# Kernel optimization log

Measured on AMD Instinct MI355X. Metric: run time of the kernel, lower is better.

## Reference

```python
import jax, jax.numpy as jnp
import numpy as np

N = 100000
IN_C = 256
HID = 128


def setup_inputs() -> dict:
    key = jax.random.key(0)
    ks = jax.random.split(key, 8)
    x = jax.random.normal(ks[0], (N, IN_C), dtype=jnp.float32)
    edge_index = jax.random.randint(ks[1], (2, 1600000), 0, N, dtype=jnp.int64)
    # GCNConv: lin (bias=False) + separate additive bias
    W1 = jax.random.normal(ks[2], (IN_C, HID), dtype=jnp.float32) / np.sqrt(IN_C)
    b1 = jnp.zeros((HID,), dtype=jnp.float32)
    W2 = jax.random.normal(ks[3], (HID, HID // 2), dtype=jnp.float32) / np.sqrt(HID)
    b2 = jnp.zeros((HID // 2,), dtype=jnp.float32)
    Wfc = jax.random.normal(ks[4], (HID // 2, 2), dtype=jnp.float32) / np.sqrt(HID // 2)
    bfc = jnp.zeros((2,), dtype=jnp.float32)
    return {"x": x, "edge_index": edge_index, "W1": W1, "b1": b1,
            "W2": W2, "b2": b2, "Wfc": Wfc, "bfc": bfc}


def _gcn_norm(edge_index, n):
    # add self-loops, symmetric normalization (PyG gcn_norm defaults)
    loop = jnp.arange(n, dtype=edge_index.dtype)
    src = jnp.concatenate([edge_index[0], loop])
    dst = jnp.concatenate([edge_index[1], loop])
    deg = jax.ops.segment_sum(jnp.ones_like(src, dtype=jnp.float32), dst,
                              num_segments=n)
    dinv = jnp.where(deg > 0, jax.lax.rsqrt(deg), 0.0)
    norm = dinv[src] * dinv[dst]  # [E + N]
    return src, dst, norm


def _gcn_conv(x, W, b, src, dst, norm, n):
    h = x @ W                       # [N, out] dense transform first
    msg = h[src] * norm[:, None]    # irregular gather, [E+N, out]
    out = jax.ops.segment_sum(msg, dst, num_segments=n)  # scatter-add
    return out + b


def reference(x, edge_index, W1, b1, W2, b2, Wfc, bfc):
    n = x.shape[0]
    src, dst, norm = _gcn_norm(edge_index, n)
    h = jax.nn.relu(_gcn_conv(x, W1, b1, src, dst, norm, n))
    # dropout is identity in eval mode
    h = jax.nn.relu(_gcn_conv(h, W2, b2, src, dst, norm, n))
    logits = h @ Wfc + bfc  # [N, 2]
    return jax.nn.log_softmax(logits, axis=1)
```

## Files before the change

### kernel.cpp

```cpp
#include <hip/hip_runtime.h>
#include <math.h>

#define IN_C 256
#define HID 128
#define H2  64
#define CAP 64

typedef __attribute__((ext_vector_type(8))) short bf16x8;
typedef __attribute__((ext_vector_type(4))) float f32x4;

__device__ __forceinline__ unsigned short f2bf(float f) {
  union { float f; unsigned int u; } v; v.f = f;
  unsigned int r = v.u + 0x7FFFu + ((v.u >> 16) & 1u);
  return (unsigned short)(r >> 16);
}
__device__ __forceinline__ float bf_lo(unsigned int u) {
  union { unsigned int u; float f; } v; v.u = u << 16; return v.f;
}
__device__ __forceinline__ float bf_hi(unsigned int u) {
  union { unsigned int u; float f; } v; v.u = u & 0xffff0000u; return v.f;
}
__device__ __forceinline__ unsigned int pack_bf(float lo, float hi) {
  return (unsigned int)f2bf(lo) | ((unsigned int)f2bf(hi) << 16);
}

__global__ void wcast_kernel(const float* __restrict__ W, unsigned short* __restrict__ Wt,
                             int K, int N) {
  int idx = blockIdx.x * 256 + threadIdx.x;
  if (idx < K * N) {
    int nn = idx / K, kk = idx % K;
    Wt[idx] = f2bf(W[kk * N + nn]);
  }
}

__global__ void dinv_kernel(const int* __restrict__ fill, float* __restrict__ dinv, int n) {
  int i = blockIdx.x * 256 + threadIdx.x;
  if (i < n) dinv[i] = rsqrtf((float)(fill[i] + 1));
}

template <int K, int N, int BM, int WM, int WN, bool A_BF16, bool SCALE>
__device__ __forceinline__ void gemm_body(const void* __restrict__ Av,
                                          const unsigned short* __restrict__ Bt,
                                          const float* __restrict__ dinv,
                                          unsigned short* __restrict__ C, int M,
                                          int bidx, short* As, short* Bs) {
  constexpr int WTM = BM / WM;
  constexpr int WTN = N / WN;
  constexpr int MB = WTM / 16, NB = WTN / 16;
  constexpr int ACH = BM * 4 / 256;
  constexpr int BCH = N * 4 / 256;

  int tid = threadIdx.x;
  int lane = tid & 63, wid = tid >> 6;
  int ln15 = lane & 15, kg = lane >> 4;
  int wm = wid / WN, wn = wid % WN;
  int row0 = bidx * BM;

  f32x4 acc[MB][NB];
#pragma unroll
  for (int i = 0; i < MB; ++i)
#pragma unroll
    for (int j = 0; j < NB; ++j) acc[i][j] = (f32x4)0.0f;

  for (int k0 = 0; k0 < K; k0 += 32) {
#pragma unroll
    for (int p = 0; p < ACH; ++p) {
      int c = p * 256 + tid;
      int row = c >> 2, kc = c & 3;
      int grow = row0 + row;
      if (A_BF16) {
        const unsigned short* Ab = (const unsigned short*)Av;
        uint4 v = make_uint4(0, 0, 0, 0);
        if (grow < M) v = *reinterpret_cast<const uint4*>(&Ab[(size_t)grow * K + k0 + kc * 8]);
        *reinterpret_cast<uint4*>(&As[row * 40 + kc * 8]) = v;
      } else {
        const float* A = (const float*)Av;
        float4 v0 = make_float4(0.f, 0.f, 0.f, 0.f), v1 = v0;
        if (grow < M) {
          const float4* ap = reinterpret_cast<const float4*>(&A[(size_t)grow * K + k0 + kc * 8]);
          v0 = ap[0]; v1 = ap[1];
        }
        bf16x8 w;
        w[0] = (short)f2bf(v0.x); w[1] = (short)f2bf(v0.y);
        w[2] = (short)f2bf(v0.z); w[3] = (short)f2bf(v0.w);
        w[4] = (short)f2bf(v1.x); w[5] = (short)f2bf(v1.y);
        w[6] = (short)f2bf(v1.z); w[7] = (short)f2bf(v1.w);
        *reinterpret_cast<bf16x8*>(&As[row * 40 + kc * 8]) = w;
      }
    }
#pragma unroll
    for (int p = 0; p < BCH; ++p) {
      int c = p * 256 + tid;
      int nrow = c >> 2, kc = c & 3;
      *reinterpret_cast<uint4*>(&Bs[nrow * 40 + kc * 8]) =
          *reinterpret_cast<const uint4*>(&Bt[(size_t)nrow * K + k0 + kc * 8]);
    }
    __syncthreads();
    bf16x8 af[MB], bfr[NB];
#pragma unroll
    for (int mb = 0; mb < MB; ++mb)
      af[mb] = *reinterpret_cast<const bf16x8*>(&As[(wm * WTM + mb * 16 + ln15) * 40 + kg * 8]);
#pragma unroll
    for (int nb = 0; nb < NB; ++nb)
      bfr[nb] = *reinterpret_cast<const bf16x8*>(&Bs[(wn * WTN + nb * 16 + ln15) * 40 + kg * 8]);
#pragma unroll
    for (int mb = 0; mb < MB; ++mb)
#pragma unroll
      for (int nb = 0; nb < NB; ++nb)
        acc[mb][nb] = __builtin_amdgcn_mfma_f32_16x16x32_bf16(af[mb], bfr[nb], acc[mb][nb], 0, 0, 0);
    __syncthreads();
  }
#pragma unroll
  for (int mb = 0; mb < MB; ++mb)
#pragma unroll
    for (int nb = 0; nb < NB; ++nb) {
      int gcol = wn * WTN + nb * 16 + ln15;
#pragma unroll
      for (int q = 0; q < 4; ++q) {
        int grow = row0 + wm * WTM + mb * 16 + kg * 4 + q;
        if (grow < M) {
          float v = acc[mb][nb][q];
          if (SCALE) v *= dinv[grow];
          C[(size_t)grow * N + gcol] = f2bf(v);
        }
      }
    }
}

__global__ __launch_bounds__(256) void fused_g1_place(
    const float* __restrict__ x, const unsigned short* __restrict__ W1T,
    unsigned short* __restrict__ h1lin, int M,
    const int* __restrict__ src, const int* __restrict__ dst, int E,
    int* __restrict__ fill, int* __restrict__ col, int GB, int PB) {
  __shared__ short smem[(64 + HID) * 40];
  int bid = blockIdx.x;
  int gp = GB < PB ? GB : PB;
  int m2 = 2 * gp;
  bool isPlace; int idx;
  if (bid < m2) { isPlace = (bid & 1); idx = bid >> 1; }
  else          { isPlace = (PB > GB); idx = gp + (bid - m2); }

  if (!isPlace) {
    gemm_body<IN_C, HID, 64, 2, 2, false, false>(x, W1T, nullptr, h1lin, M, idx,
                                                 smem, smem + 64 * 40);
  } else {
    int tid = threadIdx.x;
    int base = idx * 1024;
    int ee[4], dd[4], ss[4], sl[4]; bool ok[4];
#pragma unroll
    for (int j = 0; j < 4; ++j) { ee[j] = base + j * 256 + tid; ok[j] = ee[j] < E; }
#pragma unroll
    for (int j = 0; j < 4; ++j) {
      dd[j] = ok[j] ? dst[ee[j]] : 0;
      ss[j] = ok[j] ? src[ee[j]] : 0;
    }
#pragma unroll
    for (int j = 0; j < 4; ++j)
      sl[j] = ok[j] ? atomicAdd(&fill[dd[j]], 1) : CAP;
#pragma unroll
    for (int j = 0; j < 4; ++j)
      if (ok[j] && sl[j] < CAP) col[(size_t)dd[j] * CAP + sl[j]] = ss[j];
  }
}

__global__ __launch_bounds__(256) void gemm2_kernel(const unsigned short* __restrict__ A,
                                                    const unsigned short* __restrict__ Bt,
                                                    unsigned short* __restrict__ C, int M) {
  __shared__ short smem[(64 + H2) * 40];
  gemm_body<HID, H2, 64, 2, 2, true, false>(A, Bt, nullptr, C, M, blockIdx.x,
                                            smem, smem + 64 * 40);
}

__global__ __launch_bounds__(256) void agg1_kernel(const uint2* __restrict__ hs,
    const int* __restrict__ fill, const int* __restrict__ col,
    const float* __restrict__ dinv, const float* __restrict__ bias,
    uint2* __restrict__ outb, int n) {
  int sub = threadIdx.x >> 5, l = threadIdx.x & 31;
  int i = blockIdx.x * 8 + sub;
  if (i >= n) return;
  float di = dinv[i];
  int cnt = fill[i]; cnt = cnt > CAP ? CAP : cnt;
  const int* cp = col + (size_t)i * CAP;
  uint2 us = hs[(size_t)i * 32 + l];
  float a0 = di * bf_lo(us.x), a1 = di * bf_hi(us.x);
  float a2 = di * bf_lo(us.y), a3 = di * bf_hi(us.y);
  int k = 0;
  for (; k + 7 < cnt; k += 8) {
    int c[8]; float w[8]; uint2 u[8];
#pragma unroll
    for (int j = 0; j < 8; ++j) c[j] = cp[k + j];
#pragma unroll
    for (int j = 0; j < 8; ++j) { w[j] = dinv[c[j]]; u[j] = hs[(size_t)c[j] * 32 + l]; }
#pragma unroll
    for (int j = 0; j < 8; ++j) {
      a0 += w[j] * bf_lo(u[j].x); a1 += w[j] * bf_hi(u[j].x);
      a2 += w[j] * bf_lo(u[j].y); a3 += w[j] * bf_hi(u[j].y);
    }
  }
  for (; k + 3 < cnt; k += 4) {
    int c[4]; float w[4]; uint2 u[4];
#pragma unroll
    for (int j = 0; j < 4; ++j) c[j] = cp[k + j];
#pragma unroll
    for (int j = 0; j < 4; ++j) { w[j] = dinv[c[j]]; u[j] = hs[(size_t)c[j] * 32 + l]; }
#pragma unroll
    for (int j = 0; j < 4; ++j) {
      a0 += w[j] * bf_lo(u[j].x); a1 += w[j] * bf_hi(u[j].x);
      a2 += w[j] * bf_lo(u[j].y); a3 += w[j] * bf_hi(u[j].y);
    }
  }
  for (; k < cnt; ++k) {
    int c = cp[k]; float w = dinv[c];
    uint2 u = hs[(size_t)c * 32 + l];
    a0 += w * bf_lo(u.x); a1 += w * bf_hi(u.x);
    a2 += w * bf_lo(u.y); a3 += w * bf_hi(u.y);
  }
  float4 b = reinterpret_cast<const float4*>(bias)[l];
  a0 = di * fmaxf(di * a0 + b.x, 0.f);
  a1 = di * fmaxf(di * a1 + b.y, 0.f);
  a2 = di * fmaxf(di * a2 + b.z, 0.f);
  a3 = di * fmaxf(di * a3 + b.w, 0.f);
  uint2 o; o.x = pack_bf(a0, a1); o.y = pack_bf(a2, a3);
  outb[(size_t)i * 32 + l] = o;
}

__global__ __launch_bounds__(256) void agg2fc_kernel(const uint2* __restrict__ hs,
    const int* __restrict__ fill, const int* __restrict__ col,
    const float* __restrict__ dinv, const float* __restrict__ bias,
    const float* __restrict__ Wfc, const float* __restrict__ bfc,
    float* __restrict__ out, int n) {
  int sub = threadIdx.x >> 4, l = threadIdx.x & 15;
  int i = blockIdx.x * 16 + sub;
  if (i >= n) return;
  float di = dinv[i];
  int cnt = fill[i]; cnt = cnt > CAP ? CAP : cnt;
  const int* cp = col + (size_t)i * CAP;
  uint2 us = hs[(size_t)i * 16 + l];
  float a0 = bf_lo(us.x), a1 = bf_hi(us.x), a2 = bf_lo(us.y), a3 = bf_hi(us.y);
  int k = 0;
  for (; k + 7 < cnt; k += 8) {
    int c[8]; uint2 u[8];
#pragma unroll
    for (int j = 0; j < 8; ++j) c[j] = cp[k + j];
#pragma unroll
    for (int j = 0; j < 8; ++j) u[j] = hs[(size_t)c[j] * 16 + l];
#pragma unroll
    for (int j = 0; j < 8; ++j) {
      a0 += bf_lo(u[j].x); a1 += bf_hi(u[j].x);
      a2 += bf_lo(u[j].y); a3 += bf_hi(u[j].y);
    }
  }
  for (; k + 1 < cnt; k += 2) {
    uint2 u0 = hs[(size_t)cp[k] * 16 + l];
    uint2 u1 = hs[(size_t)cp[k + 1] * 16 + l];
    a0 += bf_lo(u0.x) + bf_lo(u1.x); a1 += bf_hi(u0.x) + bf_hi(u1.x);
    a2 += bf_lo(u0.y) + bf_lo(u1.y); a3 += bf_hi(u0.y) + bf_hi(u1.y);
  }
  if (k < cnt) {
    uint2 u = hs[(size_t)cp[k] * 16 + l];
    a0 += bf_lo(u.x); a1 += bf_hi(u.x); a2 += bf_lo(u.y); a3 += bf_hi(u.y);
  }
  float4 b = reinterpret_cast<const float4*>(bias)[l];
  a0 = fmaxf(di * a0 + b.x, 0.f);
  a1 = fmaxf(di * a1 + b.y, 0.f);
  a2 = fmaxf(di * a2 + b.z, 0.f);
  a3 = fmaxf(di * a3 + b.w, 0.f);
  float4 w01 = reinterpret_cast<const float4*>(Wfc)[2 * l];
  float4 w23 = reinterpret_cast<const float4*>(Wfc)[2 * l + 1];
  float p0 = a0 * w01.x + a1 * w01.z + a2 * w23.x + a3 * w23.z;
  float p1 = a0 * w01.y + a1 * w01.w + a2 * w23.y + a3 * w23.w;
#pragma unroll
  for (int off = 8; off; off >>= 1) {
    p0 += __shfl_xor(p0, off, 16);
    p1 += __shfl_xor(p1, off, 16);
  }
  if (l == 0) {
    float l0 = p0 + bfc[0], l1 = p1 + bfc[1];
    float m = fmaxf(l0, l1);
    float lse = m + logf(expf(l0 - m) + expf(l1 - m));
    float2 o; o.x = l0 - lse; o.y = l1 - lse;
    reinterpret_cast<float2*>(out)[i] = o;
  }
}

extern "C" void kernel_launch(void* const* d_in, const int* in_sizes, int n_in,
                              void* d_out, int out_size, void* d_ws, size_t ws_size,
                              hipStream_t stream) {
  const float* x   = (const float*)d_in[0];
  const int*   ei  = (const int*)d_in[1];
  const float* W1  = (const float*)d_in[2];
  const float* b1  = (const float*)d_in[3];
  const float* W2  = (const float*)d_in[4];
  const float* b2  = (const float*)d_in[5];
  const float* Wfc = (const float*)d_in[6];
  const float* bfc = (const float*)d_in[7];
  float* out = (float*)d_out;

  int n = in_sizes[0] / IN_C;
  int E = in_sizes[1] / 2;
  const int* src = ei;
  const int* dst = ei + E;

  char* ws = (char*)d_ws;
  size_t off = 0;
  auto alloc = [&](size_t bytes) {
    void* p = ws + off;
    off = (off + bytes + 255) & ~(size_t)255;
    return p;
  };
  int*   fill   = (int*)alloc((size_t)n * 4);
  float* dinv   = (float*)alloc((size_t)n * 4);
  int*   col    = (int*)alloc((size_t)n * CAP * 4);
  unsigned short* h1lin = (unsigned short*)alloc((size_t)n * HID * 2);
  unsigned short* h1    = (unsigned short*)alloc((size_t)n * HID * 2);
  unsigned short* h2lin = (unsigned short*)alloc((size_t)n * H2 * 2);
  unsigned short* W1T   = (unsigned short*)alloc((size_t)IN_C * HID * 2);
  unsigned short* W2T   = (unsigned short*)alloc((size_t)HID * H2 * 2);

  hipMemsetAsync(fill, 0, (size_t)n * 4, stream);
  wcast_kernel<<<(IN_C * HID + 255) / 256, 256, 0, stream>>>(W1, W1T, IN_C, HID);
  wcast_kernel<<<(HID * H2 + 255) / 256, 256, 0, stream>>>(W2, W2T, HID, H2);

  int GB = (n + 63) / 64;
  int PB = (E + 1023) / 1024;
  fused_g1_place<<<GB + PB, 256, 0, stream>>>(x, W1T, h1lin, n, src, dst, E, fill, col, GB, PB);

  dinv_kernel<<<(n + 255) / 256, 256, 0, stream>>>(fill, dinv, n);
  agg1_kernel<<<(n + 7) / 8, 256, 0, stream>>>((const uint2*)h1lin, fill, col, dinv, b1, (uint2*)h1, n);
  gemm2_kernel<<<(n + 63) / 64, 256, 0, stream>>>(h1, W2T, h2lin, n);
  agg2fc_kernel<<<(n + 15) / 16, 256, 0, stream>>>((const uint2*)h2lin, fill, col, dinv, b2, Wfc, bfc, out, n);
}
```

Before: 196.0 us.

## Widen aggregation loads to 16B, inline dinv, rebalance GEMM/placement block mix

Both aggregation kernels now read eight bf16 values per lane with uint4 loads, using half as many lanes per node and twice as many nodes per block. The separate dinv kernel and its buffer are removed; each node's normalization is computed on the fly as rsqrt(fill+1), including for every neighbour. The fused GEMM1 and edge-placement launch now interleaves four GEMM blocks with one placement block, and each placement block handles 4096 edges. The intent is fewer launches, wider memory transactions and better overlap of the atomic-heavy placement with the GEMM, at the cost of an extra gathered fill load and rsqrt per neighbour.

```diff
diff --git a/kernel.cpp b/kernel.cpp
--- a/kernel.cpp
+++ b/kernel.cpp
@@ -22,6 +22,18 @@
 }
 __device__ __forceinline__ unsigned int pack_bf(float lo, float hi) {
   return (unsigned int)f2bf(lo) | ((unsigned int)f2bf(hi) << 16);
+}
+__device__ __forceinline__ void add8w(float* a, uint4 u, float w) {
+  a[0] += w * bf_lo(u.x); a[1] += w * bf_hi(u.x);
+  a[2] += w * bf_lo(u.y); a[3] += w * bf_hi(u.y);
+  a[4] += w * bf_lo(u.z); a[5] += w * bf_hi(u.z);
+  a[6] += w * bf_lo(u.w); a[7] += w * bf_hi(u.w);
+}
+__device__ __forceinline__ void add8(float* a, uint4 u) {
+  a[0] += bf_lo(u.x); a[1] += bf_hi(u.x);
+  a[2] += bf_lo(u.y); a[3] += bf_hi(u.y);
+  a[4] += bf_lo(u.z); a[5] += bf_hi(u.z);
+  a[6] += bf_lo(u.w); a[7] += bf_hi(u.w);
 }
 
 __global__ void wcast_kernel(const float* __restrict__ W, unsigned short* __restrict__ Wt,
@@ -33,15 +45,9 @@
   }
 }
 
-__global__ void dinv_kernel(const int* __restrict__ fill, float* __restrict__ dinv, int n) {
-  int i = blockIdx.x * 256 + threadIdx.x;
-  if (i < n) dinv[i] = rsqrtf((float)(fill[i] + 1));
-}
-
-template <int K, int N, int BM, int WM, int WN, bool A_BF16, bool SCALE>
+template <int K, int N, int BM, int WM, int WN, bool A_BF16>
 __device__ __forceinline__ void gemm_body(const void* __restrict__ Av,
                                           const unsigned short* __restrict__ Bt,
-                                          const float* __restrict__ dinv,
                                           unsigned short* __restrict__ C, int M,
                                           int bidx, short* As, short* Bs) {
   constexpr int WTM = BM / WM;
@@ -118,11 +124,7 @@
 #pragma unroll
       for (int q = 0; q < 4; ++q) {
         int grow = row0 + wm * WTM + mb * 16 + kg * 4 + q;
-        if (grow < M) {
-          float v = acc[mb][nb][q];
-          if (SCALE) v *= dinv[grow];
-          C[(size_t)grow * N + gcol] = f2bf(v);
-        }
+        if (grow < M) C[(size_t)grow * N + gcol] = f2bf(acc[mb][nb][q]);
       }
     }
 }
@@ -134,31 +136,29 @@
     int* __restrict__ fill, int* __restrict__ col, int GB, int PB) {
   __shared__ short smem[(64 + HID) * 40];
   int bid = blockIdx.x;
-  int gp = GB < PB ? GB : PB;
-  int m2 = 2 * gp;
-  bool isPlace; int idx;
-  if (bid < m2) { isPlace = (bid & 1); idx = bid >> 1; }
-  else          { isPlace = (PB > GB); idx = gp + (bid - m2); }
-
+  bool isPlace = (bid % 5 == 4);
   if (!isPlace) {
-    gemm_body<IN_C, HID, 64, 2, 2, false, false>(x, W1T, nullptr, h1lin, M, idx,
-                                                 smem, smem + 64 * 40);
+    int idx = bid - bid / 5;
+    if (idx < GB)
+      gemm_body<IN_C, HID, 64, 2, 2, false>(x, W1T, h1lin, M, idx, smem, smem + 64 * 40);
   } else {
+    int idx = bid / 5;
+    if (idx >= PB) return;
     int tid = threadIdx.x;
-    int base = idx * 1024;
-    int ee[4], dd[4], ss[4], sl[4]; bool ok[4];
-#pragma unroll
-    for (int j = 0; j < 4; ++j) { ee[j] = base + j * 256 + tid; ok[j] = ee[j] < E; }
-#pragma unroll
-    for (int j = 0; j < 4; ++j) {
-      dd[j] = ok[j] ? dst[ee[j]] : 0;
-      ss[j] = ok[j] ? src[ee[j]] : 0;
+    int base = idx * 4096;
+    int dd[16], ss[16], sl[16]; bool ok[16];
+#pragma unroll
+    for (int j = 0; j < 16; ++j) {
+      int e = base + j * 256 + tid;
+      ok[j] = e < E;
+      dd[j] = ok[j] ? dst[e] : 0;
+      ss[j] = ok[j] ? src[e] : 0;
     }
 #pragma unroll
-    for (int j = 0; j < 4; ++j)
+    for (int j = 0; j < 16; ++j)
       sl[j] = ok[j] ? atomicAdd(&fill[dd[j]], 1) : CAP;
 #pragma unroll
-    for (int j = 0; j < 4; ++j)
+    for (int j = 0; j < 16; ++j)
       if (ok[j] && sl[j] < CAP) col[(size_t)dd[j] * CAP + sl[j]] = ss[j];
   }
 }
@@ -167,112 +167,124 @@
                                                     const unsigned short* __restrict__ Bt,
                                                     unsigned short* __restrict__ C, int M) {
   __shared__ short smem[(64 + H2) * 40];
-  gemm_body<HID, H2, 64, 2, 2, true, false>(A, Bt, nullptr, C, M, blockIdx.x,
-                                            smem, smem + 64 * 40);
-}
-
-__global__ __launch_bounds__(256) void agg1_kernel(const uint2* __restrict__ hs,
+  gemm_body<HID, H2, 64, 2, 2, true>(A, Bt, C, M, blockIdx.x, smem, smem + 64 * 40);
+}
+
+__global__ __launch_bounds__(256) void agg1_kernel(const uint4* __restrict__ hs4,
     const int* __restrict__ fill, const int* __restrict__ col,
-    const float* __restrict__ dinv, const float* __restrict__ bias,
-    uint2* __restrict__ outb, int n) {
-  int sub = threadIdx.x >> 5, l = threadIdx.x & 31;
-  int i = blockIdx.x * 8 + sub;
-  if (i >= n) return;
-  float di = dinv[i];
-  int cnt = fill[i]; cnt = cnt > CAP ? CAP : cnt;
-  const int* cp = col + (size_t)i * CAP;
-  uint2 us = hs[(size_t)i * 32 + l];
-  float a0 = di * bf_lo(us.x), a1 = di * bf_hi(us.x);
-  float a2 = di * bf_lo(us.y), a3 = di * bf_hi(us.y);
-  int k = 0;
-  for (; k + 7 < cnt; k += 8) {
-    int c[8]; float w[8]; uint2 u[8];
-#pragma unroll
-    for (int j = 0; j < 8; ++j) c[j] = cp[k + j];
-#pragma unroll
-    for (int j = 0; j < 8; ++j) { w[j] = dinv[c[j]]; u[j] = hs[(size_t)c[j] * 32 + l]; }
-#pragma unroll
-    for (int j = 0; j < 8; ++j) {
-      a0 += w[j] * bf_lo(u[j].x); a1 += w[j] * bf_hi(u[j].x);
-      a2 += w[j] * bf_lo(u[j].y); a3 += w[j] * bf_hi(u[j].y);
-    }
-  }
-  for (; k + 3 < cnt; k += 4) {
-    int c[4]; float w[4]; uint2 u[4];
-#pragma unroll
-    for (int j = 0; j < 4; ++j) c[j] = cp[k + j];
-#pragma unroll
-    for (int j = 0; j < 4; ++j) { w[j] = dinv[c[j]]; u[j] = hs[(size_t)c[j] * 32 + l]; }
-#pragma unroll
-    for (int j = 0; j < 4; ++j) {
-      a0 += w[j] * bf_lo(u[j].x); a1 += w[j] * bf_hi(u[j].x);
-      a2 += w[j] * bf_lo(u[j].y); a3 += w[j] * bf_hi(u[j].y);
-    }
-  }
-  for (; k < cnt; ++k) {
-    int c = cp[k]; float w = dinv[c];
-    uint2 u = hs[(size_t)c * 32 + l];
-    a0 += w * bf_lo(u.x); a1 += w * bf_hi(u.x);
-    a2 += w * bf_lo(u.y); a3 += w * bf_hi(u.y);
-  }
-  float4 b = reinterpret_cast<const float4*>(bias)[l];
-  a0 = di * fmaxf(di * a0 + b.x, 0.f);
-  a1 = di * fmaxf(di * a1 + b.y, 0.f);
-  a2 = di * fmaxf(di * a2 + b.z, 0.f);
-  a3 = di * fmaxf(di * a3 + b.w, 0.f);
-  uint2 o; o.x = pack_bf(a0, a1); o.y = pack_bf(a2, a3);
-  outb[(size_t)i * 32 + l] = o;
-}
-
-__global__ __launch_bounds__(256) void agg2fc_kernel(const uint2* __restrict__ hs,
-    const int* __restrict__ fill, const int* __restrict__ col,
-    const float* __restrict__ dinv, const float* __restrict__ bias,
-    const float* __restrict__ Wfc, const float* __restrict__ bfc,
-    float* __restrict__ out, int n) {
+    const float* __restrict__ bias, uint4* __restrict__ outb, int n) {
   int sub = threadIdx.x >> 4, l = threadIdx.x & 15;
   int i = blockIdx.x * 16 + sub;
   if (i >= n) return;
-  float di = dinv[i];
-  int cnt = fill[i]; cnt = cnt > CAP ? CAP : cnt;
+  int degi = fill[i];
+  float di = rsqrtf((float)(degi + 1));
+  int cnt = degi > CAP ? CAP : degi;
   const int* cp = col + (size_t)i * CAP;
-  uint2 us = hs[(size_t)i * 16 + l];
-  float a0 = bf_lo(us.x), a1 = bf_hi(us.x), a2 = bf_lo(us.y), a3 = bf_hi(us.y);
+  float a[8];
+  uint4 us = hs4[(size_t)i * 16 + l];
+  a[0] = di * bf_lo(us.x); a[1] = di * bf_hi(us.x);
+  a[2] = di * bf_lo(us.y); a[3] = di * bf_hi(us.y);
+  a[4] = di * bf_lo(us.z); a[5] = di * bf_hi(us.z);
+  a[6] = di * bf_lo(us.w); a[7] = di * bf_hi(us.w);
   int k = 0;
   for (; k + 7 < cnt; k += 8) {
-    int c[8]; uint2 u[8];
+    int c[8], f[8]; uint4 u[8];
 #pragma unroll
     for (int j = 0; j < 8; ++j) c[j] = cp[k + j];
 #pragma unroll
-    for (int j = 0; j < 8; ++j) u[j] = hs[(size_t)c[j] * 16 + l];
-#pragma unroll
-    for (int j = 0; j < 8; ++j) {
-      a0 += bf_lo(u[j].x); a1 += bf_hi(u[j].x);
-      a2 += bf_lo(u[j].y); a3 += bf_hi(u[j].y);
-    }
-  }
-  for (; k + 1 < cnt; k += 2) {
-    uint2 u0 = hs[(size_t)cp[k] * 16 + l];
-    uint2 u1 = hs[(size_t)cp[k + 1] * 16 + l];
-    a0 += bf_lo(u0.x) + bf_lo(u1.x); a1 += bf_hi(u0.x) + bf_hi(u1.x);
-    a2 += bf_lo(u0.y) + bf_lo(u1.y); a3 += bf_hi(u0.y) + bf_hi(u1.y);
-  }
-  if (k < cnt) {
-    uint2 u = hs[(size_t)cp[k] * 16 + l];
-    a0 += bf_lo(u.x); a1 += bf_hi(u.x); a2 += bf_lo(u.y); a3 += bf_hi(u.y);
-  }
-  float4 b = reinterpret_cast<const float4*>(bias)[l];
-  a0 = fmaxf(di * a0 + b.x, 0.f);
-  a1 = fmaxf(di * a1 + b.y, 0.f);
-  a2 = fmaxf(di * a2 + b.z, 0.f);
-  a3 = fmaxf(di * a3 + b.w, 0.f);
-  float4 w01 = reinterpret_cast<const float4*>(Wfc)[2 * l];
-  float4 w23 = reinterpret_cast<const float4*>(Wfc)[2 * l + 1];
-  float p0 = a0 * w01.x + a1 * w01.z + a2 * w23.x + a3 * w23.z;
-  float p1 = a0 * w01.y + a1 * w01.w + a2 * w23.y + a3 * w23.w;
-#pragma unroll
-  for (int off = 8; off; off >>= 1) {
-    p0 += __shfl_xor(p0, off, 16);
-    p1 += __shfl_xor(p1, off, 16);
+    for (int j = 0; j < 8; ++j) { f[j] = fill[c[j]]; u[j] = hs4[(size_t)c[j] * 16 + l]; }
+#pragma unroll
+    for (int j = 0; j < 8; ++j) add8w(a, u[j], rsqrtf((float)(f[j] + 1)));
+  }
+  for (; k + 3 < cnt; k += 4) {
+    int c[4], f[4]; uint4 u[4];
+#pragma unroll
+    for (int j = 0; j < 4; ++j) c[j] = cp[k + j];
+#pragma unroll
+    for (int j = 0; j < 4; ++j) { f[j] = fill[c[j]]; u[j] = hs4[(size_t)c[j] * 16 + l]; }
+#pragma unroll
+    for (int j = 0; j < 4; ++j) add8w(a, u[j], rsqrtf((float)(f[j] + 1)));
+  }
+  for (; k < cnt; ++k) {
+    int c = cp[k];
+    float w = rsqrtf((float)(fill[c] + 1));
+    add8w(a, hs4[(size_t)c * 16 + l], w);
+  }
+  float4 bA = reinterpret_cast<const float4*>(bias)[2 * l];
+  float4 bB = reinterpret_cast<const float4*>(bias)[2 * l + 1];
+  float r0 = di * fmaxf(di * a[0] + bA.x, 0.f);
+  float r1 = di * fmaxf(di * a[1] + bA.y, 0.f);
+  float r2 = di * fmaxf(di * a[2] + bA.z, 0.f);
+  float r3 = di * fmaxf(di * a[3] + bA.w, 0.f);
+  float r4 = di * fmaxf(di * a[4] + bB.x, 0.f);
+  float r5 = di * fmaxf(di * a[5] + bB.y, 0.f);
+  float r6 = di * fmaxf(di * a[6] + bB.z, 0.f);
+  float r7 = di * fmaxf(di * a[7] + bB.w, 0.f);
+  uint4 o;
+  o.x = pack_bf(r0, r1); o.y = pack_bf(r2, r3);
+  o.z = pack_bf(r4, r5); o.w = pack_bf(r6, r7);
+  outb[(size_t)i * 16 + l] = o;
+}
+
+__global__ __launch_bounds__(256) void agg2fc_kernel(const uint4* __restrict__ hs4,
+    const int* __restrict__ fill, const int* __restrict__ col,
+    const float* __restrict__ bias, const float* __restrict__ Wfc,
+    const float* __restrict__ bfc, float* __restrict__ out, int n) {
+  int sub = threadIdx.x >> 3, l = threadIdx.x & 7;
+  int i = blockIdx.x * 32 + sub;
+  if (i >= n) return;
+  int degi = fill[i];
+  float di = rsqrtf((float)(degi + 1));
+  int cnt = degi > CAP ? CAP : degi;
+  const int* cp = col + (size_t)i * CAP;
+  float a[8];
+  uint4 us = hs4[(size_t)i * 8 + l];
+  a[0] = bf_lo(us.x); a[1] = bf_hi(us.x);
+  a[2] = bf_lo(us.y); a[3] = bf_hi(us.y);
+  a[4] = bf_lo(us.z); a[5] = bf_hi(us.z);
+  a[6] = bf_lo(us.w); a[7] = bf_hi(us.w);
+  int k = 0;
+  for (; k + 7 < cnt; k += 8) {
+    int c[8]; uint4 u[8];
+#pragma unroll
+    for (int j = 0; j < 8; ++j) c[j] = cp[k + j];
+#pragma unroll
+    for (int j = 0; j < 8; ++j) u[j] = hs4[(size_t)c[j] * 8 + l];
+#pragma unroll
+    for (int j = 0; j < 8; ++j) add8(a, u[j]);
+  }
+  for (; k + 3 < cnt; k += 4) {
+    int c[4]; uint4 u[4];
+#pragma unroll
+    for (int j = 0; j < 4; ++j) c[j] = cp[k + j];
+#pragma unroll
+    for (int j = 0; j < 4; ++j) u[j] = hs4[(size_t)c[j] * 8 + l];
+#pragma unroll
+    for (int j = 0; j < 4; ++j) add8(a, u[j]);
+  }
+  for (; k < cnt; ++k) add8(a, hs4[(size_t)cp[k] * 8 + l]);
+  float4 bA = reinterpret_cast<const float4*>(bias)[2 * l];
+  float4 bB = reinterpret_cast<const float4*>(bias)[2 * l + 1];
+  float r[8];
+  r[0] = fmaxf(di * a[0] + bA.x, 0.f);
+  r[1] = fmaxf(di * a[1] + bA.y, 0.f);
+  r[2] = fmaxf(di * a[2] + bA.z, 0.f);
+  r[3] = fmaxf(di * a[3] + bA.w, 0.f);
+  r[4] = fmaxf(di * a[4] + bB.x, 0.f);
+  r[5] = fmaxf(di * a[5] + bB.y, 0.f);
+  r[6] = fmaxf(di * a[6] + bB.z, 0.f);
+  r[7] = fmaxf(di * a[7] + bB.w, 0.f);
+  float p0 = 0.f, p1 = 0.f;
+#pragma unroll
+  for (int s = 0; s < 4; ++s) {
+    float4 w = reinterpret_cast<const float4*>(Wfc)[4 * l + s];
+    p0 += r[2 * s] * w.x + r[2 * s + 1] * w.z;
+    p1 += r[2 * s] * w.y + r[2 * s + 1] * w.w;
+  }
+#pragma unroll
+  for (int off = 4; off; off >>= 1) {
+    p0 += __shfl_xor(p0, off, 8);
+    p1 += __shfl_xor(p1, off, 8);
   }
   if (l == 0) {
     float l0 = p0 + bfc[0], l1 = p1 + bfc[1];
@@ -309,7 +321,6 @@
     return p;
   };
   int*   fill   = (int*)alloc((size_t)n * 4);
-  float* dinv   = (float*)alloc((size_t)n * 4);
   int*   col    = (int*)alloc((size_t)n * CAP * 4);
   unsigned short* h1lin = (unsigned short*)alloc((size_t)n * HID * 2);
   unsigned short* h1    = (unsigned short*)alloc((size_t)n * HID * 2);
@@ -322,11 +333,11 @@
   wcast_kernel<<<(HID * H2 + 255) / 256, 256, 0, stream>>>(W2, W2T, HID, H2);
 
   int GB = (n + 63) / 64;
-  int PB = (E + 1023) / 1024;
-  fused_g1_place<<<GB + PB, 256, 0, stream>>>(x, W1T, h1lin, n, src, dst, E, fill, col, GB, PB);
-
-  dinv_kernel<<<(n + 255) / 256, 256, 0, stream>>>(fill, dinv, n);
-  agg1_kernel<<<(n + 7) / 8, 256, 0, stream>>>((const uint2*)h1lin, fill, col, dinv, b1, (uint2*)h1, n);
+  int PB = (E + 4095) / 4096;
+  if (4 * PB < GB) PB = (GB + 3) / 4;
+  fused_g1_place<<<5 * PB, 256, 0, stream>>>(x, W1T, h1lin, n, src, dst, E, fill, col, GB, PB);
+
+  agg1_kernel<<<(n + 15) / 16, 256, 0, stream>>>((const uint4*)h1lin, fill, col, b1, (uint4*)h1, n);
   gemm2_kernel<<<(n + 63) / 64, 256, 0, stream>>>(h1, W2T, h2lin, n);
-  agg2fc_kernel<<<(n + 15) / 16, 256, 0, stream>>>((const uint2*)h2lin, fill, col, dinv, b2, Wfc, bfc, out, n);
-}
+  agg2fc_kernel<<<(n + 31) / 32, 256, 0, stream>>>((const uint4*)h2lin, fill, col, b2, Wfc, bfc, out, n);
+}
```

Result: slower. 218.5 us (+11.5%).
